# Kernel tuning notes

Measured on AMD Instinct MI355X. Metric: run time of the kernel, lower is better.

The kernel has to match this reference:

```python
import jax, jax.numpy as jnp
import numpy as np

AZ = -999999.0  # ALMOST_ZERO_LOG_SCALE
N = 100000      # nodes
E = N - 1       # tree edges
D = 768         # input_dim
H = 256         # hidden_dim
C = 16          # num_classes


def setup_inputs() -> dict:
    key = jax.random.key(0)
    ks = jax.random.split(key, 14)
    scale = 0.02
    features = jax.random.normal(ks[0], (N, D), dtype=jnp.float32)
    # tree edges: child i (1..N-1) has parent sampled from [0, N)
    parent_idx = jax.random.randint(ks[1], (E,), 0, N, dtype=jnp.int32)
    child_idx = jnp.arange(1, N, dtype=jnp.int32)
    label_observed = jax.random.randint(ks[2], (N,), 0, 2, dtype=jnp.int32)
    true_labels = jax.random.randint(ks[3], (N,), 0, C, dtype=jnp.int32)
    # MLP feature extractor (num_layers=2, Linear+ReLU each, feature_extractor=True)
    W1 = jax.random.normal(ks[4], (D, H), dtype=jnp.float32) * scale
    b1 = jnp.zeros((H,), dtype=jnp.float32)
    W2 = jax.random.normal(ks[5], (H, H), dtype=jnp.float32) * scale
    b2 = jnp.zeros((H,), dtype=jnp.float32)
    # build_unary_potentials: Linear(H, C)
    Wu = jax.random.normal(ks[6], (H, C), dtype=jnp.float32) * scale
    bu = jnp.zeros((C,), dtype=jnp.float32)
    # build_edge_potentials: Linear(2H, C*C)
    We = jax.random.normal(ks[7], (2 * H, C * C), dtype=jnp.float32) * scale
    be = jnp.zeros((C * C,), dtype=jnp.float32)
    return {
        "features": features, "parent_idx": parent_idx, "child_idx": child_idx,
        "label_observed": label_observed, "true_labels": true_labels,
        "W1": W1, "b1": b1, "W2": W2, "b2": b2,
        "Wu": Wu, "bu": bu, "We": We, "be": be,
    }


def reference(features, parent_idx, child_idx, label_observed, true_labels,
              W1, b1, W2, b2, Wu, bu, We, be):
    obs = label_observed.astype(bool)
    # MLP feature extractor over all nodes at once (original loops per-node)
    h = jax.nn.relu(features @ W1 + b1)
    h = jax.nn.relu(h @ W2 + b2)                      # [N, H]
    # unary potentials; observed nodes get 0 at true label, AZ elsewhere
    unary_pred = h @ Wu + bu                          # [N, C]
    lbl = jnp.arange(C, dtype=true_labels.dtype)
    obs_unary = jnp.where(true_labels[:, None] == lbl[None, :], 0.0, AZ)
    unary = jnp.where(obs[:, None], obs_unary, unary_pred)  # [N, C]
    # edge potentials: Linear on concat(parent_hidden, child_hidden)
    hp = h[parent_idx]                                # [E, H]
    hc = h[child_idx]                                 # [E, H]
    ep = (jnp.concatenate([hp, hc], axis=1) @ We + be).reshape(E, C, C)
    pl = true_labels[parent_idx]                      # [E]
    cl = true_labels[child_idx]                       # [E]
    op = obs[parent_idx]                              # [E]
    oc = obs[child_idx]                               # [E]
    row = lbl[None, :, None]                          # broadcast over rows
    col = lbl[None, None, :]                          # broadcast over cols
    # both observed: 0 at [parent_label, child_label], AZ elsewhere
    allow_both = (row == pl[:, None, None]) & (col == cl[:, None, None])
    both = (op & oc)[:, None, None]
    # child-only observed: keep row at child label; parent-only: keep col at parent label
    keep = (((oc & ~op)[:, None, None] & (row == cl[:, None, None]))
            | ((op & ~oc)[:, None, None] & (col == pl[:, None, None]))
            | (~op & ~oc)[:, None, None])
    ep_masked = jnp.where(both,
                          jnp.where(allow_both, 0.0, AZ),
                          jnp.where(keep, ep, ep + AZ))
    return unary, ep_masked
```

## Files before the change

kernel.cpp:

```cpp
#include <hip/hip_runtime.h>
#include <cstddef>

#define AZ -999999.0f

typedef float  f32x4  __attribute__((ext_vector_type(4)));
typedef short  s16x8  __attribute__((ext_vector_type(8)));
typedef __bf16 bf16x8 __attribute__((ext_vector_type(8)));
typedef unsigned short ushort_t;

__device__ __forceinline__ unsigned short f2bf(float f) {
    union { float f; unsigned u; } un; un.f = f;
    return (unsigned short)((un.u + 0x7FFFu + ((un.u >> 16) & 1u)) >> 16);
}

__device__ __forceinline__ f32x4 mfma16(s16x8 a, s16x8 b, f32x4 c) {
    return __builtin_amdgcn_mfma_f32_16x16x32_bf16(
        __builtin_bit_cast(bf16x8, a), __builtin_bit_cast(bf16x8, b), c, 0, 0, 0);
}

__device__ __forceinline__ void gl2lds16(const void* g, void* l) {
    __builtin_amdgcn_global_load_lds(
        (const __attribute__((address_space(1))) unsigned int*)g,
        (__attribute__((address_space(3))) unsigned int*)l, 16, 0, 0);
}

__global__ void setup_kernel(
    const float* __restrict__ W1, const float* __restrict__ W2,
    const float* __restrict__ We, const float* __restrict__ Wu,
    ushort_t* __restrict__ W1T, ushort_t* __restrict__ W2T,
    ushort_t* __restrict__ WeT, ushort_t* __restrict__ WuTs,
    const int* __restrict__ pidx, const int* __restrict__ cidx,
    const int* __restrict__ tl, const int* __restrict__ obs,
    int* __restrict__ meta, int E)
{
    int b = blockIdx.x, t = threadIdx.x;
    if (b < 768) {
        int idx = b * 256 + t; int k = idx >> 8, n = idx & 255;
        W1T[(size_t)n * 768 + k] = f2bf(W1[idx]);
    } else if (b < 1024) {
        int idx = (b - 768) * 256 + t; int k = idx >> 8, n = idx & 255;
        W2T[n * 256 + k] = f2bf(W2[idx]);
    } else if (b < 1536) {
        int idx = (b - 1024) * 256 + t; int k = idx >> 8, n = idx & 255;
        WeT[(size_t)n * 512 + k] = f2bf(We[idx]);
    } else if (b < 1552) {
        int idx = (b - 1536) * 256 + t; int k = idx >> 4, c = idx & 15;
        WuTs[c * 256 + (((k >> 3) ^ (c & 7)) << 3) + (k & 7)] = f2bf(Wu[idx]);
    } else {
        int e = (b - 1552) * 256 + t;
        if (e < E) {
            int p = pidx[e], c = cidx[e];
            meta[e] = (tl[p] & 15) | ((tl[c] & 15) << 4)
                    | ((obs[p] & 1) << 8) | ((obs[c] & 1) << 9);
        }
    }
}

template<int AMODE, int EPI>
__global__ __launch_bounds__(256) void gemm_kernel(
    const void* __restrict__ Aptr, const ushort_t* __restrict__ BT,
    const float* __restrict__ bias, void* __restrict__ outp,
    int M, int K,
    const int* __restrict__ parent_idx, const int* __restrict__ child_idx,
    const int* __restrict__ meta)
{
    constexpr int ABYTES = (AMODE == 0) ? 16384 : 8192;
    __shared__ __align__(16) char smem[ABYTES + 8192];
    float*    Asf = (float*)smem;
    ushort_t* Ash = (ushort_t*)smem;
    ushort_t* Bsh = (ushort_t*)(smem + ABYTES);

    const int tid  = threadIdx.x;
    const int lane = tid & 63, wave = tid >> 6;
    const int row0    = blockIdx.y * 128;
    const int colbase = blockIdx.x * 128;
    const int wr = (wave >> 1) * 64, wc = (wave & 1) * 64;
    const int quad = lane >> 4, l16 = lane & 15;

    const int sub4 = lane >> 2, c4 = lane & 3;
    const int gcB  = c4 ^ ((sub4 >> 1) & 3);
    size_t b_off[2]; unsigned lds_b[2];
#pragma unroll
    for (int j = 0; j < 2; ++j) {
        int r = wave * 32 + j * 16 + sub4;
        b_off[j] = (size_t)(colbase + r) * K + gcB * 8;
        lds_b[j] = (unsigned)(wave * 32 + j * 16) * 64;
    }
    const int sub8 = lane >> 3, c8 = lane & 7;
    size_t a_off[4]; unsigned lds_a[4];
    int pn[2], cn[2];
    if constexpr (AMODE == 0) {
        const int gcA = c8 ^ sub8;
#pragma unroll
        for (int j = 0; j < 4; ++j) {
            int r  = wave * 32 + j * 8 + sub8;
            int gr = row0 + r; if (gr > M - 1) gr = M - 1;
            a_off[j] = (size_t)gr * K + gcA * 4;
            lds_a[j] = (unsigned)(wave * 32 + j * 8) * 128;
        }
    } else {
        const int gcA = c4 ^ ((sub4 >> 1) & 3);
#pragma unroll
        for (int j = 0; j < 2; ++j) {
            int r  = wave * 32 + j * 16 + sub4;
            int gr = row0 + r; if (gr > M - 1) gr = M - 1;
            if constexpr (AMODE == 2) { pn[j] = parent_idx[gr]; cn[j] = child_idx[gr]; }
            a_off[j] = (size_t)gr * K + gcA * 8;
            lds_a[j] = (unsigned)(wave * 32 + j * 16) * 64;
        }
        if constexpr (AMODE == 2) { a_off[0] = gcA * 8; a_off[1] = gcA * 8; }
    }

    const f32x4 fz = {0.f, 0.f, 0.f, 0.f};
    f32x4 acc[4][4];
#pragma unroll
    for (int i = 0; i < 4; ++i)
#pragma unroll
        for (int j = 0; j < 4; ++j) acc[i][j] = fz;

    const ushort_t* Abh = (const ushort_t*)Aptr;
    const float*    Af  = (const float*)Aptr;

    const int nkt = K >> 5;
    for (int kt = 0; kt < nkt; ++kt) {
        const int kbase = kt << 5;
        if constexpr (AMODE == 0) {
#pragma unroll
            for (int j = 0; j < 4; ++j)
                gl2lds16(Af + a_off[j] + kbase, smem + lds_a[j]);
        } else {
#pragma unroll
            for (int j = 0; j < 2; ++j) {
                int node = (kbase < 256) ? pn[j] : cn[j];
                gl2lds16(Abh + (size_t)node * 256 + (kbase & 255) + a_off[j],
                         smem + lds_a[j]);
            }
        }
#pragma unroll
        for (int j = 0; j < 2; ++j)
            gl2lds16(BT + b_off[j] + kbase, (char*)Bsh + lds_b[j]);

        __syncthreads();

        s16x8 af[4], bf[4];
        if constexpr (AMODE == 0) {
            const int s = l16 & 7;
            const int c0 = (2 * quad) ^ s, c1 = c0 ^ 1;
#pragma unroll
            for (int f = 0; f < 4; ++f) {
                int row = wr + f * 16 + l16;
                f32x4 v0 = *(const f32x4*)&Asf[row * 32 + c0 * 4];
                f32x4 v1 = *(const f32x4*)&Asf[row * 32 + c1 * 4];
                s16x8 a;
                a[0] = (short)f2bf(v0[0]); a[1] = (short)f2bf(v0[1]);
                a[2] = (short)f2bf(v0[2]); a[3] = (short)f2bf(v0[3]);
                a[4] = (short)f2bf(v1[0]); a[5] = (short)f2bf(v1[1]);
                a[6] = (short)f2bf(v1[2]); a[7] = (short)f2bf(v1[3]);
                af[f] = a;
            }
        } else {
            const int ca = quad ^ ((l16 >> 1) & 3);
#pragma unroll
            for (int f = 0; f < 4; ++f)
                af[f] = *(const s16x8*)&Ash[(wr + f * 16 + l16) * 32 + ca * 8];
        }
        {
            const int cb = quad ^ ((l16 >> 1) & 3);
#pragma unroll
            for (int f = 0; f < 4; ++f)
                bf[f] = *(const s16x8*)&Bsh[(wc + f * 16 + l16) * 32 + cb * 8];
        }
#pragma unroll
        for (int fr = 0; fr < 4; ++fr)
#pragma unroll
            for (int fc = 0; fc < 4; ++fc)
                acc[fr][fc] = mfma16(af[fr], bf[fc], acc[fr][fc]);
        __syncthreads();
    }

    float bv[4];
#pragma unroll
    for (int fc = 0; fc < 4; ++fc) bv[fc] = bias[colbase + wc + fc * 16 + l16];

    if constexpr (EPI == 0) {
        ushort_t* out = (ushort_t*)outp;
#pragma unroll
        for (int fr = 0; fr < 4; ++fr) {
#pragma unroll
            for (int r = 0; r < 4; ++r) {
                int gr = row0 + wr + fr * 16 + quad * 4 + r;
                if (gr < M) {
#pragma unroll
                    for (int fc = 0; fc < 4; ++fc) {
                        float v = acc[fr][fc][r] + bv[fc];
                        v = v > 0.f ? v : 0.f;
                        out[(size_t)gr * 256 + colbase + wc + fc * 16 + l16] = f2bf(v);
                    }
                }
            }
        }
    } else {
        float* out = (float*)outp;
#pragma unroll
        for (int fr = 0; fr < 4; ++fr) {
#pragma unroll
            for (int r = 0; r < 4; ++r) {
                int e = row0 + wr + fr * 16 + quad * 4 + r;
                if (e < M) {
                    int m  = meta[e];
                    int pl = m & 15, cl = (m >> 4) & 15;
                    int op = (m >> 8) & 1, oc = (m >> 9) & 1;
#pragma unroll
                    for (int fc = 0; fc < 4; ++fc) {
                        int n = colbase + wc + fc * 16 + l16;
                        float v = acc[fr][fc][r] + bv[fc];
                        int rr = n >> 4, cc = n & 15;
                        if (op & oc)  v = (rr == pl && cc == cl) ? 0.0f : AZ;
                        else if (oc)  { if (rr != cl) v += AZ; }
                        else if (op)  { if (cc != pl) v += AZ; }
                        out[(size_t)e * 256 + n] = v;
                    }
                }
            }
        }
    }
}

__global__ __launch_bounds__(256) void gemm2_unary_kernel(
    const ushort_t* __restrict__ h1, const ushort_t* __restrict__ W2T,
    const float* __restrict__ b2, const ushort_t* __restrict__ WuTs,
    const float* __restrict__ bu, const int* __restrict__ tl,
    const int* __restrict__ obs, ushort_t* __restrict__ h2,
    float* __restrict__ out_unary, int N)
{
    __shared__ __align__(16) char smem[4096 + 16384 + 32768 + 8192];
    ushort_t* Ash = (ushort_t*)smem;
    ushort_t* Bsh = (ushort_t*)(smem + 4096);
    ushort_t* Hsh = (ushort_t*)(smem + 20480);
    ushort_t* Wsh = (ushort_t*)(smem + 53248);

    const int tid = threadIdx.x, lane = tid & 63, wave = tid >> 6;
    const int quad = lane >> 4, l16 = lane & 15;
    const int sub4 = lane >> 2, c4 = lane & 3;
    const int n0 = blockIdx.x * 64;
    const int wc = wave * 64;

#pragma unroll
    for (int j = 0; j < 2; ++j)
        gl2lds16(WuTs + j * 2048 + wave * 512 + lane * 8,
                 (char*)Wsh + j * 4096 + wave * 1024);

    const int gcA = c4 ^ ((sub4 >> 1) & 3);
    int gra = n0 + wave * 16 + sub4; if (gra > N - 1) gra = N - 1;
    const size_t a_goff = (size_t)gra * 256 + gcA * 8;
    const unsigned a_loff = (unsigned)wave * 1024;
    size_t b_goff[4]; unsigned b_loff[4];
#pragma unroll
    for (int j = 0; j < 4; ++j) {
        int nrow = j * 64 + wave * 16 + sub4;
        b_goff[j] = (size_t)nrow * 256 + gcA * 8;
        b_loff[j] = (unsigned)(j * 64 + wave * 16) * 64;
    }

    const f32x4 fz = {0.f, 0.f, 0.f, 0.f};
    f32x4 acc[4][4];
#pragma unroll
    for (int i = 0; i < 4; ++i)
#pragma unroll
        for (int j = 0; j < 4; ++j) acc[i][j] = fz;

    for (int kt = 0; kt < 8; ++kt) {
        const int kbase = kt << 5;
        gl2lds16(h1 + a_goff + kbase, smem + a_loff);
#pragma unroll
        for (int j = 0; j < 4; ++j)
            gl2lds16(W2T + b_goff[j] + kbase, (char*)Bsh + b_loff[j]);
        __syncthreads();
        const int cs = quad ^ ((l16 >> 1) & 3);
        s16x8 af[4], bf[4];
#pragma unroll
        for (int f = 0; f < 4; ++f)
            af[f] = *(const s16x8*)&Ash[(f * 16 + l16) * 32 + cs * 8];
#pragma unroll
        for (int f = 0; f < 4; ++f)
            bf[f] = *(const s16x8*)&Bsh[(wc + f * 16 + l16) * 32 + cs * 8];
#pragma unroll
        for (int fr = 0; fr < 4; ++fr)
#pragma unroll
            for (int fc = 0; fc < 4; ++fc)
                acc[fr][fc] = mfma16(af[fr], bf[fc], acc[fr][fc]);
        __syncthreads();
    }

    float bv[4];
#pragma unroll
    for (int fc = 0; fc < 4; ++fc) bv[fc] = b2[wc + fc * 16 + l16];
#pragma unroll
    for (int fr = 0; fr < 4; ++fr) {
#pragma unroll
        for (int r = 0; r < 4; ++r) {
            int row = fr * 16 + quad * 4 + r;
#pragma unroll
            for (int fc = 0; fc < 4; ++fc) {
                int col = wc + fc * 16 + l16;
                float v = acc[fr][fc][r] + bv[fc];
                v = v > 0.f ? v : 0.f;
                Hsh[row * 256 + (((col >> 3) ^ (row & 7)) << 3) + (col & 7)] = f2bf(v);
            }
        }
    }
    __syncthreads();

    {
        int row = tid >> 2, cc = tid & 3;
        int gr = n0 + row;
        if (gr < N) {
#pragma unroll
            for (int j = 0; j < 8; ++j) {
                int phys = (j * 4 + cc) ^ (row & 7);
                s16x8 v = *(const s16x8*)&Hsh[row * 256 + phys * 8];
                *(s16x8*)&h2[(size_t)gr * 256 + (j * 4 + cc) * 8] = v;
            }
        }
    }

    {
        const int arow = wave * 16 + l16;
        f32x4 accu = fz;
#pragma unroll
        for (int kt = 0; kt < 8; ++kt) {
            int pc = (kt * 4 + quad) ^ (l16 & 7);
            s16x8 a = *(const s16x8*)&Hsh[arow * 256 + pc * 8];
            s16x8 b = *(const s16x8*)&Wsh[l16 * 256 + pc * 8];
            accu = mfma16(a, b, accu);
        }
        float bvc = bu[l16];
#pragma unroll
        for (int r = 0; r < 4; ++r) {
            int node = n0 + wave * 16 + quad * 4 + r;
            if (node < N) {
                float v = obs[node] ? ((tl[node] == l16) ? 0.0f : AZ) : (accu[r] + bvc);
                out_unary[(size_t)node * 16 + l16] = v;
            }
        }
    }
}

extern "C" void kernel_launch(void* const* d_in, const int* in_sizes, int n_in,
                              void* d_out, int out_size, void* d_ws, size_t ws_size,
                              hipStream_t stream) {
    const float* features = (const float*)d_in[0];
    const int* parent_idx = (const int*)d_in[1];
    const int* child_idx  = (const int*)d_in[2];
    const int* label_obs  = (const int*)d_in[3];
    const int* true_lab   = (const int*)d_in[4];
    const float* W1 = (const float*)d_in[5];
    const float* b1 = (const float*)d_in[6];
    const float* W2 = (const float*)d_in[7];
    const float* b2 = (const float*)d_in[8];
    const float* Wu = (const float*)d_in[9];
    const float* bu = (const float*)d_in[10];
    const float* We = (const float*)d_in[11];
    const float* be = (const float*)d_in[12];
    float* out = (float*)d_out;

    const int N = 100000, E = N - 1;

    char* ws = (char*)d_ws;
    ushort_t* h1   = (ushort_t*)ws;
    ushort_t* h2   = (ushort_t*)(ws + (size_t)N * 256 * 2);
    ushort_t* W1T  = (ushort_t*)(ws + (size_t)N * 256 * 4);
    ushort_t* W2T  = W1T + 768 * 256;
    ushort_t* WeT  = W2T + 256 * 256;
    ushort_t* WuTs = WeT + 512 * 256;
    int*      meta = (int*)(WuTs + 16 * 256);

    setup_kernel<<<1943, 256, 0, stream>>>(W1, W2, We, Wu, W1T, W2T, WeT, WuTs,
                                           parent_idx, child_idx, true_lab, label_obs,
                                           meta, E);

    dim3 gn(2, (N + 127) / 128);
    gemm_kernel<0, 0><<<gn, 256, 0, stream>>>(features, W1T, b1, h1, N, 768,
                                              nullptr, nullptr, nullptr);
    gemm2_unary_kernel<<<(N + 63) / 64, 256, 0, stream>>>(h1, W2T, b2, WuTs, bu,
                                                          true_lab, label_obs, h2, out, N);
    dim3 ge(2, (E + 127) / 128);
    gemm_kernel<2, 1><<<ge, 256, 0, stream>>>(h2, WeT, be, out + (size_t)N * 16, E, 512,
                                              parent_idx, child_idx, meta);
}
```

Baseline: 642.0 us.

## Retile GEMMs to 64x256 so each block covers full output width

The GEMM kernel switches from 128x128 tiles with a 2D wave layout to 64-row by 256-column tiles, with each wave owning a 64-column slice. Each A row, whether fp32 features or gathered parent/child hidden rows, is now read once instead of once per column block, which halves A global traffic. The grid doubles along rows and the weight tile loaded per k-step doubles, so B reuse per block shrinks. The manual float-to-bf16 rounding is also replaced by a compiler bf16 conversion.

```diff
diff --git a/kernel.cpp b/kernel.cpp
--- a/kernel.cpp
+++ b/kernel.cpp
@@ -8,9 +8,8 @@
 typedef __bf16 bf16x8 __attribute__((ext_vector_type(8)));
 typedef unsigned short ushort_t;
 
-__device__ __forceinline__ unsigned short f2bf(float f) {
-    union { float f; unsigned u; } un; un.f = f;
-    return (unsigned short)((un.u + 0x7FFFu + ((un.u >> 16) & 1u)) >> 16);
+__device__ __forceinline__ ushort_t f2bf(float f) {
+    return __builtin_bit_cast(ushort_t, (__bf16)f);
 }
 
 __device__ __forceinline__ f32x4 mfma16(s16x8 a, s16x8 b, f32x4 c) {
@@ -64,51 +63,46 @@
     const int* __restrict__ parent_idx, const int* __restrict__ child_idx,
     const int* __restrict__ meta)
 {
-    constexpr int ABYTES = (AMODE == 0) ? 16384 : 8192;
-    __shared__ __align__(16) char smem[ABYTES + 8192];
+    constexpr int ABYTES = (AMODE == 0) ? 8192 : 4096;
+    __shared__ __align__(16) char smem[ABYTES + 16384];
     float*    Asf = (float*)smem;
     ushort_t* Ash = (ushort_t*)smem;
     ushort_t* Bsh = (ushort_t*)(smem + ABYTES);
 
     const int tid  = threadIdx.x;
     const int lane = tid & 63, wave = tid >> 6;
-    const int row0    = blockIdx.y * 128;
-    const int colbase = blockIdx.x * 128;
-    const int wr = (wave >> 1) * 64, wc = (wave & 1) * 64;
+    const int row0 = blockIdx.y * 64;
+    const int wc   = wave * 64;
     const int quad = lane >> 4, l16 = lane & 15;
-
-    const int sub4 = lane >> 2, c4 = lane & 3;
-    const int gcB  = c4 ^ ((sub4 >> 1) & 3);
-    size_t b_off[2]; unsigned lds_b[2];
-#pragma unroll
-    for (int j = 0; j < 2; ++j) {
-        int r = wave * 32 + j * 16 + sub4;
-        b_off[j] = (size_t)(colbase + r) * K + gcB * 8;
-        lds_b[j] = (unsigned)(wave * 32 + j * 16) * 64;
-    }
-    const int sub8 = lane >> 3, c8 = lane & 7;
-    size_t a_off[4]; unsigned lds_a[4];
-    int pn[2], cn[2];
+    const int c4   = lane & 3;
+
+    const int rB  = tid >> 2;
+    const int gcB = c4 ^ ((rB >> 1) & 3);
+    size_t   b_off[4]; unsigned lds_b[4];
+#pragma unroll
+    for (int j = 0; j < 4; ++j) {
+        b_off[j] = (size_t)(j * 64 + rB) * K + gcB * 8;
+        lds_b[j] = (unsigned)(j * 64 + wave * 16) * 64;
+    }
+
+    size_t a_off[2]; unsigned lds_a[2];
+    int pn = 0, cn = 0; unsigned lds_a0 = 0, a_col = 0;
     if constexpr (AMODE == 0) {
-        const int gcA = c8 ^ sub8;
-#pragma unroll
-        for (int j = 0; j < 4; ++j) {
-            int r  = wave * 32 + j * 8 + sub8;
-            int gr = row0 + r; if (gr > M - 1) gr = M - 1;
+        const int c8 = tid & 7, r8 = tid >> 3;
+        const int gcA = c8 ^ (r8 & 7);
+#pragma unroll
+        for (int j = 0; j < 2; ++j) {
+            int gr = row0 + j * 32 + r8; if (gr > M - 1) gr = M - 1;
             a_off[j] = (size_t)gr * K + gcA * 4;
-            lds_a[j] = (unsigned)(wave * 32 + j * 8) * 128;
+            lds_a[j] = (unsigned)(j * 32 + wave * 8) * 128;
         }
     } else {
-        const int gcA = c4 ^ ((sub4 >> 1) & 3);
-#pragma unroll
-        for (int j = 0; j < 2; ++j) {
-            int r  = wave * 32 + j * 16 + sub4;
-            int gr = row0 + r; if (gr > M - 1) gr = M - 1;
-            if constexpr (AMODE == 2) { pn[j] = parent_idx[gr]; cn[j] = child_idx[gr]; }
-            a_off[j] = (size_t)gr * K + gcA * 8;
-            lds_a[j] = (unsigned)(wave * 32 + j * 16) * 64;
-        }
-        if constexpr (AMODE == 2) { a_off[0] = gcA * 8; a_off[1] = gcA * 8; }
+        const int rA = tid >> 2;
+        const int gcA2 = c4 ^ ((rA >> 1) & 3);
+        int gr = row0 + rA; if (gr > M - 1) gr = M - 1;
+        pn = parent_idx[gr]; cn = child_idx[gr];
+        a_col  = gcA2 * 8;
+        lds_a0 = (unsigned)(wave * 16) * 64;
     }
 
     const f32x4 fz = {0.f, 0.f, 0.f, 0.f};
@@ -126,18 +120,15 @@
         const int kbase = kt << 5;
         if constexpr (AMODE == 0) {
 #pragma unroll
-            for (int j = 0; j < 4; ++j)
+            for (int j = 0; j < 2; ++j)
                 gl2lds16(Af + a_off[j] + kbase, smem + lds_a[j]);
         } else {
-#pragma unroll
-            for (int j = 0; j < 2; ++j) {
-                int node = (kbase < 256) ? pn[j] : cn[j];
-                gl2lds16(Abh + (size_t)node * 256 + (kbase & 255) + a_off[j],
-                         smem + lds_a[j]);
-            }
-        }
-#pragma unroll
-        for (int j = 0; j < 2; ++j)
+            int node = (kbase < 256) ? pn : cn;
+            gl2lds16(Abh + (size_t)node * 256 + (kbase & 255) + a_col,
+                     smem + lds_a0);
+        }
+#pragma unroll
+        for (int j = 0; j < 4; ++j)
             gl2lds16(BT + b_off[j] + kbase, (char*)Bsh + lds_b[j]);
 
         __syncthreads();
@@ -148,7 +139,7 @@
             const int c0 = (2 * quad) ^ s, c1 = c0 ^ 1;
 #pragma unroll
             for (int f = 0; f < 4; ++f) {
-                int row = wr + f * 16 + l16;
+                int row = f * 16 + l16;
                 f32x4 v0 = *(const f32x4*)&Asf[row * 32 + c0 * 4];
                 f32x4 v1 = *(const f32x4*)&Asf[row * 32 + c1 * 4];
                 s16x8 a;
@@ -162,7 +153,7 @@
             const int ca = quad ^ ((l16 >> 1) & 3);
 #pragma unroll
             for (int f = 0; f < 4; ++f)
-                af[f] = *(const s16x8*)&Ash[(wr + f * 16 + l16) * 32 + ca * 8];
+                af[f] = *(const s16x8*)&Ash[(f * 16 + l16) * 32 + ca * 8];
         }
         {
             const int cb = quad ^ ((l16 >> 1) & 3);
@@ -180,7 +171,7 @@
 
     float bv[4];
 #pragma unroll
-    for (int fc = 0; fc < 4; ++fc) bv[fc] = bias[colbase + wc + fc * 16 + l16];
+    for (int fc = 0; fc < 4; ++fc) bv[fc] = bias[wc + fc * 16 + l16];
 
     if constexpr (EPI == 0) {
         ushort_t* out = (ushort_t*)outp;
@@ -188,13 +179,13 @@
         for (int fr = 0; fr < 4; ++fr) {
 #pragma unroll
             for (int r = 0; r < 4; ++r) {
-                int gr = row0 + wr + fr * 16 + quad * 4 + r;
+                int gr = row0 + fr * 16 + quad * 4 + r;
                 if (gr < M) {
 #pragma unroll
                     for (int fc = 0; fc < 4; ++fc) {
                         float v = acc[fr][fc][r] + bv[fc];
                         v = v > 0.f ? v : 0.f;
-                        out[(size_t)gr * 256 + colbase + wc + fc * 16 + l16] = f2bf(v);
+                        out[(size_t)gr * 256 + wc + fc * 16 + l16] = f2bf(v);
                     }
                 }
             }
@@ -205,14 +196,14 @@
         for (int fr = 0; fr < 4; ++fr) {
 #pragma unroll
             for (int r = 0; r < 4; ++r) {
-                int e = row0 + wr + fr * 16 + quad * 4 + r;
+                int e = row0 + fr * 16 + quad * 4 + r;
                 if (e < M) {
                     int m  = meta[e];
                     int pl = m & 15, cl = (m >> 4) & 15;
                     int op = (m >> 8) & 1, oc = (m >> 9) & 1;
 #pragma unroll
                     for (int fc = 0; fc < 4; ++fc) {
-                        int n = colbase + wc + fc * 16 + l16;
+                        int n = wc + fc * 16 + l16;
                         float v = acc[fr][fc][r] + bv[fc];
                         int rr = n >> 4, cc = n & 15;
                         if (op & oc)  v = (rr == pl && cc == cl) ? 0.0f : AZ;
@@ -379,12 +370,12 @@
                                            parent_idx, child_idx, true_lab, label_obs,
                                            meta, E);
 
-    dim3 gn(2, (N + 127) / 128);
+    dim3 gn(1, (N + 63) / 64);
     gemm_kernel<0, 0><<<gn, 256, 0, stream>>>(features, W1T, b1, h1, N, 768,
                                               nullptr, nullptr, nullptr);
     gemm2_unary_kernel<<<(N + 63) / 64, 256, 0, stream>>>(h1, W2T, b2, WuTs, bu,
                                                           true_lab, label_obs, h2, out, N);
-    dim3 ge(2, (E + 127) / 128);
+    dim3 ge(1, (E + 63) / 64);
     gemm_kernel<2, 1><<<ge, 256, 0, stream>>>(h2, WeT, be, out + (size_t)N * 16, E, 512,
                                               parent_idx, child_idx, meta);
 }
```

Result: faster. 615.8 us (-4.1%).
